# Performance work log

Hardware: AMD Instinct MI355X
Metric: run time of the kernel (lower is better)

## Reference

```python
import jax, jax.numpy as jnp
import numpy as np

LMBDA = 100.0
GAMMA = 0.5
EPS_EV = 1e-10


def _safe_evals(e):
    return jnp.clip(jnp.nan_to_num(e, nan=EPS_EV, posinf=1e6, neginf=EPS_EV), EPS_EV, None)


def get_mask(evals1, evals2, gamma):
    # evals1, evals2: [B, K]; returns D: [B, K, K] with D[b,i,j] from (evals2[b,i], evals1[b,j])
    e1 = _safe_evals(evals1)
    e2 = _safe_evals(evals2)
    scale = jnp.clip(jnp.maximum(e1.max(axis=1), e2.max(axis=1)), 1e-10, None)[:, None]
    e1 = e1 / scale
    e2 = e2 / scale
    g1 = e1 ** gamma  # [B,K] -> broadcast as column index j
    g2 = e2 ** gamma  # [B,K] -> broadcast as row index i
    d1 = g1 * g1 + 1.0
    d2 = g2 * g2 + 1.0
    M_re = (g2 / d2)[:, :, None] - (g1 / d1)[:, None, :]
    M_im = (1.0 / d2)[:, :, None] - (1.0 / d1)[:, None, :]
    return jnp.nan_to_num(M_re * M_re + M_im * M_im, nan=0.0, posinf=1e6, neginf=0.0)


def setup_inputs() -> dict:
    key = jax.random.key(0)
    k = jax.random.split(key, 6)
    B, N, K, C = 8, 20000, 128, 256
    return {
        "feat_x": jax.random.normal(k[0], (B, N, C), dtype=jnp.float32),
        "feat_y": jax.random.normal(k[1], (B, N, C), dtype=jnp.float32),
        "evals_x": jax.random.uniform(k[2], (B, K), dtype=jnp.float32),
        "evals_y": jax.random.uniform(k[3], (B, K), dtype=jnp.float32),
        "evecs_trans_x": jax.random.normal(k[4], (B, K, N), dtype=jnp.float32),
        "evecs_trans_y": jax.random.normal(k[5], (B, K, N), dtype=jnp.float32),
    }


def reference(feat_x, feat_y, evals_x, evals_y, evecs_trans_x, evecs_trans_y):
    # Spectral projection of features: [B,K,N] @ [B,N,C] -> [B,K,C]
    A = jnp.einsum('bkn,bnc->bkc', evecs_trans_x, feat_x)
    Bm = jnp.einsum('bkn,bnc->bkc', evecs_trans_y, feat_y)
    D = get_mask(evals_x, evals_y, GAMMA)  # [B,K,K]

    A_A_t = jnp.einsum('bic,bjc->bij', A, A)   # [B,K,K]
    B_A_t = jnp.einsum('bic,bjc->bij', Bm, A)  # [B,K,K]

    K = A.shape[1]
    eye = jnp.eye(K, dtype=A.dtype)
    # lhs[b,i] = A_A_t[b] + lmbda * diag(D[b,i]) + 1e-8 * I  -> [B,K,K,K]
    lhs = A_A_t[:, None, :, :] + LMBDA * (D[..., None] * eye) + 1e-8 * eye
    rhs = B_A_t[..., None]  # [B,K,K,1]; rhs[b,i] = B_A_t[b,i,:]
    Cxy = jnp.linalg.solve(lhs, rhs)[..., 0]  # [B,K,K]; row i of Cxy = solution for eigenvalue i
    return Cxy
```

## Files before the change

kernel.cpp:

```cpp
#include <hip/hip_runtime.h>
#include <math.h>

#define B_ 8
#define N_ 20000
#define K_ 128
#define C_ 256

static_assert(N_ % 32 == 0, "N must be multiple of 32");

constexpr float LMBDA = 100.0f;
constexpr float EPS_EV = 1e-10f;

typedef unsigned int u32x4 __attribute__((ext_vector_type(4)));
typedef short short8_t __attribute__((ext_vector_type(8)));
typedef float f32x4 __attribute__((ext_vector_type(4)));

static __device__ inline void split2(float x0, float x1, unsigned& h, unsigned& l) {
  unsigned u0 = __builtin_bit_cast(unsigned, x0);
  unsigned u1 = __builtin_bit_cast(unsigned, x1);
  h = __builtin_amdgcn_perm(u1, u0, 0x07060302u);
  float r0 = x0 - __builtin_bit_cast(float, u0 & 0xFFFF0000u);
  float r1 = x1 - __builtin_bit_cast(float, u1 & 0xFFFF0000u);
  unsigned v0 = __builtin_bit_cast(unsigned, r0);
  unsigned v1 = __builtin_bit_cast(unsigned, r1);
  v0 += 0x7FFFu + ((v0 >> 16) & 1u);
  v1 += 0x7FFFu + ((v1 >> 16) & 1u);
  l = __builtin_amdgcn_perm(v1, v0, 0x07060302u);
}

__global__ __launch_bounds__(512, 2)
void proj_mfma(const float* __restrict__ feat_x, const float* __restrict__ feat_y,
               const float* __restrict__ evx, const float* __restrict__ evy,
               float* __restrict__ part, int Sa, int chunk) {
  const int bm = blockIdx.z;
  const int b = bm >> 1, mat = bm & 1;
  const float* __restrict__ E = (mat ? evy : evx) + (size_t)b * K_ * N_;
  const float* __restrict__ F = (mat ? feat_y : feat_x) + (size_t)b * N_ * C_;
  const int c0 = blockIdx.x << 7;
  const int s = blockIdx.y;
  const int nb = s * chunk;
  const int ne = min(N_, nb + chunk);
  const int nt = (ne - nb) >> 5;

  __shared__ unsigned short Ah[128][40];
  __shared__ unsigned short Al[128][40];
  __shared__ unsigned short Bh[128][40];
  __shared__ unsigned short Bl[128][40];

  const int t = threadIdx.x;
  const int lane = t & 63, wv = t >> 6;
  const int wm = wv & 3;
  const int wcc = wv >> 2;
  const int lr = lane & 15, lg = lane >> 4;
  const int k0 = lg << 3;

  const int am = t >> 2, ak = (t & 3) << 3;
  const int cl = t & 127, gq = (t >> 7) << 2;

  f32x4 acc[2][4];
#pragma unroll
  for (int i = 0; i < 2; ++i)
#pragma unroll
    for (int j = 0; j < 4; ++j) acc[i][j] = (f32x4){0.f, 0.f, 0.f, 0.f};

  struct Stage { float4 a0, a1; float b0, b1, b2, b3, b4, b5, b6, b7; };

  auto LOAD = [&](Stage& st, int n0) {
    const float* ep = E + (size_t)am * N_ + n0 + ak;
    st.a0 = *(const float4*)ep;
    st.a1 = *(const float4*)(ep + 4);
    const float* fp = F + (size_t)(n0 + gq) * C_ + c0 + cl;
    st.b0 = fp[0];
    st.b1 = fp[C_];
    st.b2 = fp[2 * C_];
    st.b3 = fp[3 * C_];
    const float* fp2 = fp + (size_t)16 * C_;
    st.b4 = fp2[0];
    st.b5 = fp2[C_];
    st.b6 = fp2[2 * C_];
    st.b7 = fp2[3 * C_];
  };

  auto WRITE = [&](Stage& st) {
    unsigned h01, l01, h23, l23, h45, l45, h67, l67;
    split2(st.a0.x, st.a0.y, h01, l01);
    split2(st.a0.z, st.a0.w, h23, l23);
    split2(st.a1.x, st.a1.y, h45, l45);
    split2(st.a1.z, st.a1.w, h67, l67);
    *(u32x4*)&Ah[am][ak] = (u32x4){h01, h23, h45, h67};
    *(u32x4*)&Al[am][ak] = (u32x4){l01, l23, l45, l67};
    split2(st.b0, st.b1, h01, l01);
    split2(st.b2, st.b3, h23, l23);
    *(uint2*)&Bh[cl][gq] = (uint2){h01, h23};
    *(uint2*)&Bl[cl][gq] = (uint2){l01, l23};
    split2(st.b4, st.b5, h45, l45);
    split2(st.b6, st.b7, h67, l67);
    *(uint2*)&Bh[cl][gq + 16] = (uint2){h45, h67};
    *(uint2*)&Bl[cl][gq + 16] = (uint2){l45, l67};
  };

  auto COMPUTE = [&]() {
    short8_t a_h[2], a_l[2];
#pragma unroll
    for (int mt = 0; mt < 2; ++mt) {
      const int m = (wm << 5) + (mt << 4) + lr;
      a_h[mt] = *(const short8_t*)&Ah[m][k0];
      a_l[mt] = *(const short8_t*)&Al[m][k0];
    }
#pragma unroll
    for (int ct = 0; ct < 4; ++ct) {
      const int c = (wcc << 6) + (ct << 4) + lr;
      const short8_t b_h = *(const short8_t*)&Bh[c][k0];
      const short8_t b_l = *(const short8_t*)&Bl[c][k0];
#pragma unroll
      for (int mt = 0; mt < 2; ++mt) {
        acc[mt][ct] = __builtin_amdgcn_mfma_f32_16x16x32_bf16(a_h[mt], b_h, acc[mt][ct], 0, 0, 0);
        acc[mt][ct] = __builtin_amdgcn_mfma_f32_16x16x32_bf16(a_l[mt], b_h, acc[mt][ct], 0, 0, 0);
        acc[mt][ct] = __builtin_amdgcn_mfma_f32_16x16x32_bf16(a_h[mt], b_l, acc[mt][ct], 0, 0, 0);
      }
    }
  };

  Stage sA, sB;
  LOAD(sA, nb);
  if (nt > 1) LOAD(sB, nb + 32);

  for (int it = 0; it < nt; it += 2) {
    __syncthreads();
    WRITE(sA);
    if (it + 2 < nt) LOAD(sA, nb + ((it + 2) << 5));
    __syncthreads();
    COMPUTE();
    if (it + 1 < nt) {
      __syncthreads();
      WRITE(sB);
      if (it + 3 < nt) LOAD(sB, nb + ((it + 3) << 5));
      __syncthreads();
      COMPUTE();
    }
  }

  float* __restrict__ P = part + ((size_t)bm * Sa + s) * (K_ * C_);
#pragma unroll
  for (int mt = 0; mt < 2; ++mt)
#pragma unroll
    for (int ct = 0; ct < 4; ++ct) {
      const int ccol = c0 + (wcc << 6) + (ct << 4) + lr;
#pragma unroll
      for (int r = 0; r < 4; ++r) {
        const int mrow = (wm << 5) + (mt << 4) + (lg << 2) + r;
        P[(size_t)mrow * C_ + ccol] = acc[mt][ct][r];
      }
    }
}

__global__ void reduce_parts(const float* __restrict__ part, float* __restrict__ AB, int Sa) {
  const int idx4 = blockIdx.x * 256 + threadIdx.x;
  if (idx4 >= 16 * K_ * C_ / 4) return;
  const int per = K_ * C_ / 4;
  const int bm = idx4 / per;
  const int rem4 = idx4 - bm * per;
  float4 v = {0.f, 0.f, 0.f, 0.f};
  for (int s = 0; s < Sa; ++s) {
    const float4 p = *(const float4*)&part[((size_t)bm * Sa + s) * (K_ * C_) + rem4 * 4];
    v.x += p.x; v.y += p.y; v.z += p.z; v.w += p.w;
  }
  *(float4*)&AB[(size_t)idx4 * 4] = v;
}

__global__ __launch_bounds__(256)
void gram_kernel(const float* __restrict__ AB, float* __restrict__ Sm, float* __restrict__ Rm) {
  const int b = blockIdx.x, which = blockIdx.y, qz = blockIdx.z;
  const int iq = (qz & 1) << 6, jq = (qz >> 1) << 6;
  const float* __restrict__ L  = AB + ((size_t)(b * 2 + which)) * (K_ * C_);
  const float* __restrict__ Ar = AB + ((size_t)(b * 2)) * (K_ * C_);
  float* __restrict__ out = (which ? Rm : Sm) + (size_t)b * (K_ * K_);
  const int t = threadIdx.x;
  const int ir = iq + ((t >> 4) << 2), jc = jq + ((t & 15) << 2);
  float acc[4][4] = {};
  for (int c0 = 0; c0 < C_; c0 += 4) {
    float4 li[4], rj[4];
#pragma unroll
    for (int i = 0; i < 4; ++i) li[i] = *(const float4*)(L + (size_t)(ir + i) * C_ + c0);
#pragma unroll
    for (int j = 0; j < 4; ++j) rj[j] = *(const float4*)(Ar + (size_t)(jc + j) * C_ + c0);
#pragma unroll
    for (int i = 0; i < 4; ++i)
#pragma unroll
      for (int j = 0; j < 4; ++j)
        acc[i][j] += li[i].x * rj[j].x + li[i].y * rj[j].y +
                     li[i].z * rj[j].z + li[i].w * rj[j].w;
  }
#pragma unroll
  for (int i = 0; i < 4; ++i)
#pragma unroll
    for (int j = 0; j < 4; ++j) {
      float v = acc[i][j];
      if (!which && (ir + i) == (jc + j)) v += 1e-8f;
      out[(size_t)(ir + i) * K_ + (jc + j)] = v;
    }
}

__global__ void mask_prep(const float* __restrict__ evx, const float* __restrict__ evy,
                          float* __restrict__ PQ) {
  const int b = blockIdx.x, t = threadIdx.x;
  float e1 = evx[b * K_ + t];
  float e2 = evy[b * K_ + t];
  if (e1 != e1) e1 = EPS_EV;
  if (e2 != e2) e2 = EPS_EV;
  e1 = fminf(fmaxf(e1, EPS_EV), 1e6f);
  e2 = fminf(fmaxf(e2, EPS_EV), 1e6f);

  __shared__ float wmax[2];
  float v = fmaxf(e1, e2);
#pragma unroll
  for (int d = 1; d < 64; d <<= 1) v = fmaxf(v, __shfl_xor(v, d, 64));
  if ((t & 63) == 0) wmax[t >> 6] = v;
  __syncthreads();
  const float scale = fmaxf(fmaxf(wmax[0], wmax[1]), 1e-10f);

  const float g1 = sqrtf(e1 / scale);
  const float g2 = sqrtf(e2 / scale);
  const float d1 = fmaf(g1, g1, 1.f);
  const float d2 = fmaf(g2, g2, 1.f);
  float* P = PQ + b * 512;
  P[t]       = g1 / d1;
  P[128 + t] = 1.f / d1;
  P[256 + t] = g2 / d2;
  P[384 + t] = 1.f / d2;
}

__global__ __launch_bounds__(512)
void gj_inverse(const float* __restrict__ Sm, float* __restrict__ Sinv) {
  const int b = blockIdx.x, t = threadIdx.x;
  __shared__ float a[K_ * 132];
  __shared__ float Pi[16 * 20];
  __shared__ float Rp[16 * 132];
  __shared__ float Cp[K_ * 20];
  const float* __restrict__ Sb = Sm + (size_t)b * (K_ * K_);
#pragma unroll
  for (int l = 0; l < 8; ++l) {
    int f = t + (l << 9);
    int i = f >> 5, j = (f & 31) << 2;
    *(float4*)&a[i * 132 + j] = *(const float4*)(Sb + i * K_ + j);
  }
  __syncthreads();

  const int j = t & 127, rr = t >> 7;
  const int lane = t & 63;

  for (int p = 0; p < 8; ++p) {
    const int pb = p << 4;

    if (t < 64) {
      const int r = lane & 15, g = lane >> 4;
      float4 v4 = *(const float4*)&a[(pb + r) * 132 + pb + (g << 2)];
      float vv[4] = {v4.x, v4.y, v4.z, v4.w};
#pragma unroll
      for (int k = 0; k < 16; ++k) {
        const int srcrow = (lane & 48) | k;
        float rk[4];
        rk[0] = __shfl(vv[0], srcrow);
        rk[1] = __shfl(vv[1], srcrow);
        rk[2] = __shfl(vv[2], srcrow);
        rk[3] = __shfl(vv[3], srcrow);
        const int kg = (k >> 2) << 4;
        const float pv = __shfl(vv[k & 3], kg | k);
        const float c  = __shfl(vv[k & 3], kg | r);
        const float pr = 1.0f / pv;
        float rs[4];
#pragma unroll
        for (int e = 0; e < 4; ++e) rs[e] = rk[e] * pr;
        if (r == k) {
#pragma unroll
          for (int e = 0; e < 4; ++e) vv[e] = rs[e];
          if (g == (k >> 2)) vv[k & 3] = pr;
        } else {
#pragma unroll
          for (int e = 0; e < 4; ++e) vv[e] = fmaf(-c, rs[e], vv[e]);
          if (g == (k >> 2)) vv[k & 3] = -c * pr;
        }
      }
      Pi[r * 20 + (g << 2) + 0] = vv[0];
      Pi[r * 20 + (g << 2) + 1] = vv[1];
      Pi[r * 20 + (g << 2) + 2] = vv[2];
      Pi[r * 20 + (g << 2) + 3] = vv[3];
    }
    __syncthreads();

    {
      float Ak[16];
#pragma unroll
      for (int k = 0; k < 16; ++k) Ak[k] = a[(pb + k) * 132 + j];
      const unsigned jj = (unsigned)(j - pb);
      const int r0 = rr << 2;
#pragma unroll
      for (int q = 0; q < 4; ++q) {
        const int r = r0 + q;
        float acc = 0.f;
#pragma unroll
        for (int k = 0; k < 16; ++k) acc = fmaf(Pi[r * 20 + k], Ak[k], acc);
        Rp[r * 132 + j] = (jj < 16u) ? Pi[r * 20 + jj] : acc;
      }
      const int i = j;
      const int cb = rr << 2;
      float4 cA = *(const float4*)&a[i * 132 + pb + cb];
      *(float4*)&Cp[i * 20 + cb] = cA;
    }
    __syncthreads();

    {
      float Rk[16];
#pragma unroll
      for (int k = 0; k < 16; ++k) Rk[k] = Rp[k * 132 + j];
      const unsigned jj = (unsigned)(j - pb);
      const int i0 = rr << 5;
#pragma unroll 4
      for (int m = 0; m < 32; ++m) {
        const int i = i0 + m;
        const float4 c0 = *(const float4*)&Cp[i * 20];
        const float4 c1 = *(const float4*)&Cp[i * 20 + 4];
        const float4 c2 = *(const float4*)&Cp[i * 20 + 8];
        const float4 c3 = *(const float4*)&Cp[i * 20 + 12];
        float u0 = c0.x * Rk[0] + c0.y * Rk[1] + c0.z * Rk[2] + c0.w * Rk[3];
        float u1 = c1.x * Rk[4] + c1.y * Rk[5] + c1.z * Rk[6] + c1.w * Rk[7];
        float u2 = c2.x * Rk[8] + c2.y * Rk[9] + c2.z * Rk[10] + c2.w * Rk[11];
        float u3 = c3.x * Rk[12] + c3.y * Rk[13] + c3.z * Rk[14] + c3.w * Rk[15];
        const float upd = (u0 + u1) + (u2 + u3);
        const unsigned ii = (unsigned)(i - pb);
        float newv;
        if (ii < 16u) {
          newv = Rk[ii];
        } else {
          const float base = (jj < 16u) ? 0.f : a[i * 132 + j];
          newv = base - upd;
        }
        a[i * 132 + j] = newv;
      }
    }
    __syncthreads();
  }

  float* __restrict__ O = Sinv + (size_t)b * (K_ * K_);
#pragma unroll
  for (int l = 0; l < 8; ++l) {
    int f = t + (l << 9);
    int i = f >> 5, jq = (f & 31) << 2;
    *(float4*)(O + i * K_ + jq) = *(const float4*)&a[i * 132 + jq];
  }
}

__global__ __launch_bounds__(256)
void solve_iter(const float* __restrict__ Rm, const float* __restrict__ Sinv,
                const float* __restrict__ PQ, const float* __restrict__ Xin,
                float* __restrict__ Xout, const int first) {
  const int bb = blockIdx.x;
  const int b = bb >> 2, rb = (bb & 3) << 5;
  const int t = threadIdx.x;
  __shared__ float Tt[32][34];
  __shared__ float Sv[32][132];
  __shared__ float q1[K_], p1[K_], q2l[32], p2l[32];
  {
    const float* P = PQ + b * 512;
    if (t < K_) { q1[t] = P[t]; p1[t] = P[128 + t]; }
    if (t < 32) { q2l[t] = P[256 + rb + t]; p2l[t] = P[384 + rb + t]; }
  }
  __syncthreads();
  const float* __restrict__ Rb = Rm + (size_t)b * (K_ * K_);
  const float* __restrict__ Xb = Xin + (size_t)b * (K_ * K_);
  const float* __restrict__ Si = Sinv + (size_t)b * (K_ * K_);
  const int ir = (t >> 4) << 1, jc = (t & 15) << 3;
  float acc[2][8] = {};

  for (int k0 = 0; k0 < K_; k0 += 32) {
    {
      const int i = t >> 3;
      const int kk = (t & 7) << 2;
      const int k = k0 + kk;
      const int gi = rb + i;
      float4 tv = *(const float4*)(Rb + (size_t)gi * K_ + k);
      if (!first) {
        const float4 x4 = *(const float4*)(Xb + (size_t)gi * K_ + k);
        const float qi = q2l[i], pi = p2l[i];
        float dq, dp, w;
        dq = qi - q1[k + 0]; dp = pi - p1[k + 0]; w = fmaf(dq, dq, dp * dp);
        tv.x = fmaf(-LMBDA * w, x4.x, tv.x);
        dq = qi - q1[k + 1]; dp = pi - p1[k + 1]; w = fmaf(dq, dq, dp * dp);
        tv.y = fmaf(-LMBDA * w, x4.y, tv.y);
        dq = qi - q1[k + 2]; dp = pi - p1[k + 2]; w = fmaf(dq, dq, dp * dp);
        tv.z = fmaf(-LMBDA * w, x4.z, tv.z);
        dq = qi - q1[k + 3]; dp = pi - p1[k + 3]; w = fmaf(dq, dq, dp * dp);
        tv.w = fmaf(-LMBDA * w, x4.w, tv.w);
      }
      Tt[kk + 0][i] = tv.x; Tt[kk + 1][i] = tv.y;
      Tt[kk + 2][i] = tv.z; Tt[kk + 3][i] = tv.w;
    }
#pragma unroll
    for (int l = 0; l < 4; ++l) {
      int f = t + (l << 8);
      int kk = f >> 5, j4 = (f & 31) << 2;
      *(float4*)&Sv[kk][j4] = *(const float4*)(Si + (size_t)(k0 + kk) * K_ + j4);
    }
    __syncthreads();
#pragma unroll
    for (int kk = 0; kk < 32; ++kk) {
      const float2 a2 = *(const float2*)&Tt[kk][ir];
      const float4 b0 = *(const float4*)&Sv[kk][jc];
      const float4 b1 = *(const float4*)&Sv[kk][jc + 4];
      const float bv[8] = {b0.x, b0.y, b0.z, b0.w, b1.x, b1.y, b1.z, b1.w};
#pragma unroll
      for (int jx = 0; jx < 8; ++jx) {
        acc[0][jx] = fmaf(a2.x, bv[jx], acc[0][jx]);
        acc[1][jx] = fmaf(a2.y, bv[jx], acc[1][jx]);
      }
    }
    __syncthreads();
  }

  float* __restrict__ O = Xout + (size_t)b * (K_ * K_);
#pragma unroll
  for (int i = 0; i < 2; ++i) {
    float4 o0 = {acc[i][0], acc[i][1], acc[i][2], acc[i][3]};
    float4 o1 = {acc[i][4], acc[i][5], acc[i][6], acc[i][7]};
    *(float4*)(O + (size_t)(rb + ir + i) * K_ + jc) = o0;
    *(float4*)(O + (size_t)(rb + ir + i) * K_ + jc + 4) = o1;
  }
}

extern "C" void kernel_launch(void* const* d_in, const int* in_sizes, int n_in,
                              void* d_out, int out_size, void* d_ws, size_t ws_size,
                              hipStream_t stream) {
  (void)in_sizes; (void)n_in; (void)out_size;
  const float* feat_x  = (const float*)d_in[0];
  const float* feat_y  = (const float*)d_in[1];
  const float* evals_x = (const float*)d_in[2];
  const float* evals_y = (const float*)d_in[3];
  const float* evtx    = (const float*)d_in[4];
  const float* evty    = (const float*)d_in[5];
  float* out = (float*)d_out;
  float* ws  = (float*)d_ws;

  const size_t KC16 = (size_t)16 * K_ * C_;
  const size_t KK   = (size_t)K_ * K_;
  const size_t fixed = KC16 + 3 * (KK * B_) + 4096 + 2 * (KK * B_);
  const int T = N_ / 32;

  int S = 16, Sa = 16, chunk = 0;
  for (;;) {
    int steps = (T + S - 1) / S;
    chunk = steps * 32;
    Sa = (T + steps - 1) / steps;
    if (((size_t)Sa * KC16 + fixed) * sizeof(float) <= ws_size || S == 1) break;
    S >>= 1;
  }

  float* part = ws;
  float* AB   = part + (size_t)Sa * KC16;
  float* Sm   = AB + KC16;
  float* Rm   = Sm + KK * B_;
  float* Sinv = Rm + KK * B_;
  float* PQ   = Sinv + KK * B_;
  float* X0   = PQ + 4096;
  float* X1   = X0 + KK * B_;

  mask_prep<<<dim3(8), 128, 0, stream>>>(evals_x, evals_y, PQ);
  proj_mfma<<<dim3(2, Sa, 16), 512, 0, stream>>>(feat_x, feat_y, evtx, evty, part, Sa, chunk);
  reduce_parts<<<dim3(16 * K_ * C_ / 4 / 256), 256, 0, stream>>>(part, AB, Sa);
  gram_kernel<<<dim3(8, 2, 4), 256, 0, stream>>>(AB, Sm, Rm);
  gj_inverse<<<dim3(8), 512, 0, stream>>>(Sm, Sinv);
  solve_iter<<<dim3(32), 256, 0, stream>>>(Rm, Sinv, PQ, X0, X0, 1);
  solve_iter<<<dim3(32), 256, 0, stream>>>(Rm, Sinv, PQ, X0, X1, 0);
  solve_iter<<<dim3(32), 256, 0, stream>>>(Rm, Sinv, PQ, X1, out, 0);
}
```

Measured before the change: 256.5 us.

## Double-buffer LDS tiles, swizzle B layout, and raise the occupancy bound

The projection GEMM kernel now keeps two LDS buffers for the split bf16 hi/lo tiles. The next tile is written into one buffer while MFMAs read the other, so each step needs one custom barrier (lgkmcnt wait plus s_barrier) instead of two __syncthreads. The B tile stores use an XOR swizzle of the k-slot based on the column, meant to cut LDS bank conflicts on the transposed writes and reads. The launch bound rises from 2 to 4 blocks per CU. The doubled LDS (about 80 KB per block) may keep actual occupancy at 2, while the tighter register budget risks spills.

Result: no change. 254.2 us (-0.9%).

```diff
diff --git a/kernel.cpp b/kernel.cpp
--- a/kernel.cpp
+++ b/kernel.cpp
@@ -28,7 +28,15 @@
   l = __builtin_amdgcn_perm(v1, v0, 0x07060302u);
 }
 
-__global__ __launch_bounds__(512, 2)
+#define KFENCE()                                              \
+  do {                                                        \
+    asm volatile("s_waitcnt lgkmcnt(0)" ::: "memory");        \
+    __builtin_amdgcn_sched_barrier(0);                        \
+    __builtin_amdgcn_s_barrier();                             \
+    __builtin_amdgcn_sched_barrier(0);                        \
+  } while (0)
+
+__global__ __launch_bounds__(512, 4)
 void proj_mfma(const float* __restrict__ feat_x, const float* __restrict__ feat_y,
                const float* __restrict__ evx, const float* __restrict__ evy,
                float* __restrict__ part, int Sa, int chunk) {
@@ -42,20 +50,22 @@
   const int ne = min(N_, nb + chunk);
   const int nt = (ne - nb) >> 5;
 
-  __shared__ unsigned short Ah[128][40];
-  __shared__ unsigned short Al[128][40];
-  __shared__ unsigned short Bh[128][40];
-  __shared__ unsigned short Bl[128][40];
+  __shared__ unsigned short Ah[2][128][40];
+  __shared__ unsigned short Al[2][128][40];
+  __shared__ unsigned short Bh[2][128][40];
+  __shared__ unsigned short Bl[2][128][40];
 
   const int t = threadIdx.x;
   const int lane = t & 63, wv = t >> 6;
   const int wm = wv & 3;
   const int wcc = wv >> 2;
   const int lr = lane & 15, lg = lane >> 4;
-  const int k0 = lg << 3;
 
   const int am = t >> 2, ak = (t & 3) << 3;
   const int cl = t & 127, gq = (t >> 7) << 2;
+  const int sigw = ((cl >> 3) & 3) << 1;
+  const int slotA = ((gq >> 2) ^ sigw) << 2;
+  const int slotB = (((gq >> 2) + 4) ^ sigw) << 2;
 
   f32x4 acc[2][4];
 #pragma unroll
@@ -81,37 +91,40 @@
     st.b7 = fp2[3 * C_];
   };
 
-  auto WRITE = [&](Stage& st) {
+  auto WRITE = [&](Stage& st, int p) {
     unsigned h01, l01, h23, l23, h45, l45, h67, l67;
     split2(st.a0.x, st.a0.y, h01, l01);
     split2(st.a0.z, st.a0.w, h23, l23);
     split2(st.a1.x, st.a1.y, h45, l45);
     split2(st.a1.z, st.a1.w, h67, l67);
-    *(u32x4*)&Ah[am][ak] = (u32x4){h01, h23, h45, h67};
-    *(u32x4*)&Al[am][ak] = (u32x4){l01, l23, l45, l67};
+    *(u32x4*)&Ah[p][am][ak] = (u32x4){h01, h23, h45, h67};
+    *(u32x4*)&Al[p][am][ak] = (u32x4){l01, l23, l45, l67};
     split2(st.b0, st.b1, h01, l01);
     split2(st.b2, st.b3, h23, l23);
-    *(uint2*)&Bh[cl][gq] = (uint2){h01, h23};
-    *(uint2*)&Bl[cl][gq] = (uint2){l01, l23};
+    *(uint2*)&Bh[p][cl][slotA] = (uint2){h01, h23};
+    *(uint2*)&Bl[p][cl][slotA] = (uint2){l01, l23};
     split2(st.b4, st.b5, h45, l45);
     split2(st.b6, st.b7, h67, l67);
-    *(uint2*)&Bh[cl][gq + 16] = (uint2){h45, h67};
-    *(uint2*)&Bl[cl][gq + 16] = (uint2){l45, l67};
+    *(uint2*)&Bh[p][cl][slotB] = (uint2){h45, h67};
+    *(uint2*)&Bl[p][cl][slotB] = (uint2){l45, l67};
   };
 
-  auto COMPUTE = [&]() {
+  auto COMPUTE = [&](int p) {
+    const int k0 = lg << 3;
     short8_t a_h[2], a_l[2];
 #pragma unroll
     for (int mt = 0; mt < 2; ++mt) {
       const int m = (wm << 5) + (mt << 4) + lr;
-      a_h[mt] = *(const short8_t*)&Ah[m][k0];
-      a_l[mt] = *(const short8_t*)&Al[m][k0];
+      a_h[mt] = *(const short8_t*)&Ah[p][m][k0];
+      a_l[mt] = *(const short8_t*)&Al[p][m][k0];
     }
 #pragma unroll
     for (int ct = 0; ct < 4; ++ct) {
       const int c = (wcc << 6) + (ct << 4) + lr;
-      const short8_t b_h = *(const short8_t*)&Bh[c][k0];
-      const short8_t b_l = *(const short8_t*)&Bl[c][k0];
+      const int sig = ((c >> 3) & 3) << 1;
+      const int koff = (((lg << 1) ^ sig)) << 2;
+      const short8_t b_h = *(const short8_t*)&Bh[p][c][koff];
+      const short8_t b_l = *(const short8_t*)&Bl[p][c][koff];
 #pragma unroll
       for (int mt = 0; mt < 2; ++mt) {
         acc[mt][ct] = __builtin_amdgcn_mfma_f32_16x16x32_bf16(a_h[mt], b_h, acc[mt][ct], 0, 0, 0);
@@ -124,19 +137,19 @@
   Stage sA, sB;
   LOAD(sA, nb);
   if (nt > 1) LOAD(sB, nb + 32);
+  WRITE(sA, 0);
+  KFENCE();
 
   for (int it = 0; it < nt; it += 2) {
-    __syncthreads();
-    WRITE(sA);
+    if (it + 1 < nt) WRITE(sB, 1);
     if (it + 2 < nt) LOAD(sA, nb + ((it + 2) << 5));
-    __syncthreads();
-    COMPUTE();
+    COMPUTE(0);
+    KFENCE();
     if (it + 1 < nt) {
-      __syncthreads();
-      WRITE(sB);
+      if (it + 2 < nt) WRITE(sA, 0);
       if (it + 3 < nt) LOAD(sB, nb + ((it + 3) << 5));
-      __syncthreads();
-      COMPUTE();
+      COMPUTE(1);
+      KFENCE();
     }
   }
 
```
